# Kernel optimization log

Measured on AMD Instinct MI355X. Metric: run time of the kernel, lower is better.

## Reference

```python
import jax, jax.numpy as jnp
import numpy as np

COST_CLASS, COST_BBOX, COST_GIOU = 1.0, 5.0, 2.0
NUM_FRAMES, Q_PER_FRAME, NUM_TGT, NUM_CLASSES = 36, 100, 20, 92
B = 64


def box_cxcywh_to_xyxy(b):
    cx, cy, w, h = b[..., 0], b[..., 1], b[..., 2], b[..., 3]
    return jnp.stack([cx - 0.5 * w, cy - 0.5 * h, cx + 0.5 * w, cy + 0.5 * h], axis=-1)


def pairwise_giou(b1, b2):
    # b1: [..., Q, 4], b2: [..., T, 4], xyxy -> giou [..., Q, T]
    area1 = (b1[..., 2] - b1[..., 0]) * (b1[..., 3] - b1[..., 1])
    area2 = (b2[..., 2] - b2[..., 0]) * (b2[..., 3] - b2[..., 1])
    lt = jnp.maximum(b1[..., :, None, :2], b2[..., None, :, :2])
    rb = jnp.minimum(b1[..., :, None, 2:], b2[..., None, :, 2:])
    wh = jnp.clip(rb - lt, 0.0)
    inter = wh[..., 0] * wh[..., 1]
    union = area1[..., :, None] + area2[..., None, :] - inter
    iou = inter / union
    lt_e = jnp.minimum(b1[..., :, None, :2], b2[..., None, :, :2])
    rb_e = jnp.maximum(b1[..., :, None, 2:], b2[..., None, :, 2:])
    wh_e = jnp.clip(rb_e - lt_e, 0.0)
    area_e = wh_e[..., 0] * wh_e[..., 1]
    return iou - (area_e - union) / area_e


def compute_cost(pred_logits, pred_boxes, tgt_labels, tgt_boxes):
    b = pred_logits.shape[0]
    prob = jax.nn.softmax(pred_logits.reshape(b, NUM_FRAMES, Q_PER_FRAME, -1), axis=-1)  # [B,F,Q,C]
    pb = pred_boxes.reshape(b, NUM_FRAMES, Q_PER_FRAME, 4)
    lab = jnp.transpose(tgt_labels, (1, 0, 2))            # [B,F,T]
    tb = jnp.transpose(tgt_boxes, (1, 0, 2, 3))           # [B,F,T,4]
    onehot = jax.nn.one_hot(lab, prob.shape[-1], dtype=prob.dtype)  # [B,F,T,C]
    cost_class = -jnp.einsum('bfqc,bftc->bfqt', prob, onehot)
    cost_bbox = jnp.abs(pb[:, :, :, None, :] - tb[:, :, None, :, :]).sum(-1)  # L1 cdist
    giou = pairwise_giou(box_cxcywh_to_xyxy(pb), box_cxcywh_to_xyxy(tb))
    return COST_CLASS * cost_class + COST_BBOX * cost_bbox - COST_GIOU * giou


def auction_assign(cost):
    # cost [Q, T]; returns obj_of [T]: query index assigned to each target.
    # eps-optimal auction algorithm (replaces scipy linear_sum_assignment).
    Q, T = cost.shape
    benefit = -cost.T  # [T, Q]
    spread = jnp.max(benefit) - jnp.min(benefit) + 1e-6
    eps = spread / 1000.0
    neg_inf = jnp.asarray(-1e30, cost.dtype)

    def cond(s):
        _, _, obj_of, it = s
        return jnp.logical_and(jnp.any(obj_of < 0), it < 20000)

    def body(s):
        price, owner, obj_of, it = s
        unassigned = obj_of < 0                       # [T]
        vals = benefit - price[None, :]               # [T, Q]
        top2v, top2i = jax.lax.top_k(vals, 2)
        best_obj = top2i[:, 0]                        # [T]
        bid = price[best_obj] + (top2v[:, 0] - top2v[:, 1]) + eps
        bid = jnp.where(unassigned, bid, neg_inf)
        best_bid = jnp.full((Q,), neg_inf, cost.dtype).at[best_obj].max(bid)
        pids = jnp.arange(T, dtype=jnp.int32)
        win = unassigned & (bid >= best_bid[best_obj])
        winner = jnp.full((Q,), T, jnp.int32).at[best_obj].min(jnp.where(win, pids, T))
        has_bid = winner < T
        # evict previous owners of objects that received a bid
        evict = jnp.where(has_bid & (owner >= 0), owner, T)
        obj_of = obj_of.at[evict].set(-1, mode='drop')
        qids = jnp.arange(Q, dtype=jnp.int32)
        obj_of = obj_of.at[jnp.where(has_bid, winner, T)].set(jnp.where(has_bid, qids, -1), mode='drop')
        price = jnp.where(has_bid, best_bid, price)
        owner = jnp.where(has_bid, winner, owner)
        return price, owner, obj_of, it + 1

    init = (jnp.zeros((Q,), cost.dtype), jnp.full((Q,), -1, jnp.int32),
            jnp.full((T,), -1, jnp.int32), jnp.int32(0))
    _, _, obj_of, _ = jax.lax.while_loop(cond, body, init)
    return obj_of


def setup_inputs() -> dict:
    key = jax.random.key(0)
    k1, k2, k3, k4 = jax.random.split(key, 4)
    pred_logits = jax.random.normal(k1, (B, NUM_FRAMES * Q_PER_FRAME, NUM_CLASSES), jnp.float32)
    pred_boxes = jax.random.uniform(k2, (B, NUM_FRAMES * Q_PER_FRAME, 4), jnp.float32)
    tgt_labels = jax.random.randint(k3, (NUM_FRAMES, B, NUM_TGT), 0, NUM_CLASSES, jnp.int32)
    tgt_boxes = jax.random.uniform(k4, (NUM_FRAMES, B, NUM_TGT, 4), jnp.float32)
    return {'pred_logits': pred_logits, 'pred_boxes': pred_boxes,
            'tgt_labels': tgt_labels, 'tgt_boxes': tgt_boxes}


def reference(pred_logits, pred_boxes, tgt_labels, tgt_boxes):
    cost = compute_cost(pred_logits, pred_boxes, tgt_labels, tgt_boxes)  # [B,F,Q,T]
    b, f, q, t = cost.shape
    obj_of = jax.vmap(auction_assign)(cost.reshape(b * f, q, t))  # [BF, T]
    order = jnp.argsort(obj_of, axis=-1)  # scipy returns rows ascending
    pred_idx = jnp.take_along_axis(obj_of, order, axis=-1).reshape(b, f, t)
    tgt_idx = order.astype(jnp.int32).reshape(b, f, t)
    return cost, pred_idx, tgt_idx
```

## Files before the change

kernel.cpp:

```cpp
#include <hip/hip_runtime.h>

#define NF 36
#define QN 100
#define TN 20
#define CN 92
#define NB 64
#define BSTR 112

#define TOP2_STEP(VV, IDX) do { \
    float v_ = (VV); bool c_ = v_ > v0; \
    float nv1_ = __builtin_amdgcn_fmed3f(v_, v0, v1); \
    i0 = c_ ? (IDX) : i0; v0 = fmaxf(v0, v_); v1 = nv1_; } while (0)

__global__ __launch_bounds__(64) void matcher_kernel(
    const float* __restrict__ logits,
    const float* __restrict__ pboxes,
    const int*   __restrict__ tlabels,
    const float* __restrict__ tboxes,
    float* __restrict__ out_cost,
    float* __restrict__ out_pred,
    float* __restrict__ out_tgt)
{
    const int bf = blockIdx.x;
    const int b  = bf / NF;
    const int f  = bf % NF;
    const int lane = threadIdx.x;

    __shared__ __align__(16) float ben[TN][BSTR];
    __shared__ __align__(16) float price[BSTR];
    __shared__ int   owner[QN];
    __shared__ int   bbmax[QN];
    __shared__ int   wmin[QN];
    __shared__ int   evict[TN];
    __shared__ int   objl[TN];
    __shared__ int   slab[TN];
    __shared__ float tbr[TN][4];
    __shared__ float tbx[TN][4];
    __shared__ float tarea[TN];

    if (lane < TN) {
        const int base = (f * NB + b) * TN + lane;
        slab[lane] = tlabels[base];
        const float* tb = tboxes + (size_t)base * 4;
        float cx = tb[0], cy = tb[1], w = tb[2], h = tb[3];
        tbr[lane][0] = cx; tbr[lane][1] = cy; tbr[lane][2] = w; tbr[lane][3] = h;
        float x1 = cx - 0.5f * w, y1 = cy - 0.5f * h;
        float x2 = cx + 0.5f * w, y2 = cy + 0.5f * h;
        tbx[lane][0] = x1; tbx[lane][1] = y1; tbx[lane][2] = x2; tbx[lane][3] = y2;
        tarea[lane] = (x2 - x1) * (y2 - y1);
        evict[lane] = 0;
    }
    __syncthreads();

    float mn = INFINITY, mx = -INFINITY;
    for (int p = 0; p < 2; ++p) {
        const int q = lane + 64 * p;
        if (q < QN) {
            const size_t row = (size_t)b * (NF * QN) + (size_t)f * QN + q;
            const float* L = logits + row * CN;
            const float4* L4 = reinterpret_cast<const float4*>(L);

            float g[TN];
            #pragma unroll
            for (int t = 0; t < TN; ++t) g[t] = L[slab[t]];

            float m = -INFINITY, s = 0.f;
            #pragma unroll
            for (int i = 0; i < 23; ++i) {
                float4 v = L4[i];
                float cm = fmaxf(fmaxf(v.x, v.y), fmaxf(v.z, v.w));
                float m2 = fmaxf(m, cm);
                s = s * expf(m - m2)
                  + expf(v.x - m2) + expf(v.y - m2)
                  + expf(v.z - m2) + expf(v.w - m2);
                m = m2;
            }

            float4 pbv = reinterpret_cast<const float4*>(pboxes)[row];
            float cx = pbv.x, cy = pbv.y, w = pbv.z, h = pbv.w;
            float px1 = cx - 0.5f * w, py1 = cy - 0.5f * h;
            float px2 = cx + 0.5f * w, py2 = cy + 0.5f * h;
            float a1 = (px2 - px1) * (py2 - py1);

            for (int t = 0; t < TN; ++t) {
                float pc = expf(g[t] - m) / s;
                float cb = fabsf(cx - tbr[t][0]) + fabsf(cy - tbr[t][1]);
                cb = cb + fabsf(w - tbr[t][2]);
                cb = cb + fabsf(h - tbr[t][3]);
                float ltx = fmaxf(px1, tbx[t][0]), lty = fmaxf(py1, tbx[t][1]);
                float rbx = fminf(px2, tbx[t][2]), rby = fminf(py2, tbx[t][3]);
                float wx = fmaxf(rbx - ltx, 0.f), wy = fmaxf(rby - lty, 0.f);
                float inter = wx * wy;
                float uni = a1 + tarea[t] - inter;
                float iou = inter / uni;
                float ex1 = fminf(px1, tbx[t][0]), ey1 = fminf(py1, tbx[t][1]);
                float ex2 = fmaxf(px2, tbx[t][2]), ey2 = fmaxf(py2, tbx[t][3]);
                float ew = fmaxf(ex2 - ex1, 0.f), eh = fmaxf(ey2 - ey1, 0.f);
                float ae = ew * eh;
                float giou = iou - (ae - uni) / ae;
                float cost = (-pc) + 5.0f * cb - 2.0f * giou;
                ben[t][q] = -cost;
                mn = fminf(mn, cost);
                mx = fmaxf(mx, cost);
            }
        }
    }

    for (int i = lane; i < BSTR; i += 64) price[i] = 0.f;
    for (int i = lane; i < QN; i += 64) owner[i] = -1;
    if (lane < TN) {
        float4 ninf; ninf.x = ninf.y = ninf.z = ninf.w = -INFINITY;
        float4* sp = reinterpret_cast<float4*>(&ben[lane][100]);
        sp[0] = ninf; sp[1] = ninf; sp[2] = ninf;
    }
    __syncthreads();

    #pragma unroll
    for (int off = 32; off > 0; off >>= 1) {
        mn = fminf(mn, __shfl_xor(mn, off, 64));
        mx = fmaxf(mx, __shfl_xor(mx, off, 64));
    }
    const float eps = (((-mn) - (-mx)) + 1e-6f) / 1000.0f;

    {
        float4* dst = reinterpret_cast<float4*>(out_cost + (size_t)bf * (QN * TN));
        for (int i = lane; i < (QN * TN) / 4; i += 64) {
            int k = i * 4;
            int q = k / TN, t0 = k - q * TN;
            float4 v;
            v.x = -ben[t0 + 0][q]; v.y = -ben[t0 + 1][q];
            v.z = -ben[t0 + 2][q]; v.w = -ben[t0 + 3][q];
            dst[i] = v;
        }
    }

    const int myt = lane / 3;
    const int jj  = lane - myt * 3;
    const int q0  = jj * 36;
    const bool is_leader = (lane < 60) && (jj == 0);
    float4 breg4[9];
    {
        const int tt = (lane < 60) ? myt : 0;
        const float4* bp = reinterpret_cast<const float4*>(&ben[tt][q0]);
        #pragma unroll
        for (int k = 0; k < 9; ++k) breg4[k] = bp[k];
    }
    int myobj = -1;

    for (int it = 0; it < 20000; ++it) {
        unsigned long long U = __ballot(is_leader && (myobj < 0));
        if (U == 0ull) break;
        const int u = __popcll(U);

        int bidq = 0; float bidf = 0.f;
        if (u > 2) {
            float v0 = -INFINITY, v1 = -INFINITY; int i0 = q0;
            const float4* pp = reinterpret_cast<const float4*>(&price[q0]);
            #pragma unroll
            for (int k = 0; k < 9; ++k) {
                float4 bv = breg4[k];
                float4 pv = pp[k];
                TOP2_STEP(bv.x - pv.x, q0 + 4*k + 0);
                TOP2_STEP(bv.y - pv.y, q0 + 4*k + 1);
                TOP2_STEP(bv.z - pv.z, q0 + 4*k + 2);
                TOP2_STEP(bv.w - pv.w, q0 + 4*k + 3);
            }
            {
                float av0 = __shfl_down(v0, 1), av1 = __shfl_down(v1, 1);
                int   ai0 = __shfl_down(i0, 1);
                float bv0 = __shfl_down(v0, 2), bv1 = __shfl_down(v1, 2);
                int   bi0 = __shfl_down(i0, 2);
                if (av0 > v0) { v1 = fmaxf(v0, av1); v0 = av0; i0 = ai0; }
                else          { v1 = fmaxf(av0, v1); }
                if (bv0 > v0) { v1 = fmaxf(v0, bv1); v0 = bv0; i0 = bi0; }
                else          { v1 = fmaxf(bv0, v1); }
            }
            bidq = i0;
            bidf = price[i0] + (v0 - v1) + eps;
        } else {
            const int ta = (int)__builtin_ctzll(U) / 3;
            const int tb = (u == 2) ? (int)__builtin_ctzll(U & (U - 1ull)) / 3 : ta;
            const int grp = lane >> 5;
            const int tg  = grp ? tb : ta;
            const int l   = lane & 31;
            const int lc  = (l > 25) ? 25 : l;
            const int qb  = lc * 4;
            float4 bv = *reinterpret_cast<const float4*>(&ben[tg][qb]);
            float4 pv = *reinterpret_cast<const float4*>(&price[qb]);
            float v0 = -INFINITY, v1 = -INFINITY; int i0 = qb;
            TOP2_STEP(bv.x - pv.x, qb + 0);
            TOP2_STEP(bv.y - pv.y, qb + 1);
            TOP2_STEP(bv.z - pv.z, qb + 2);
            TOP2_STEP(bv.w - pv.w, qb + 3);
            #pragma unroll
            for (int s = 16; s >= 1; s >>= 1) {
                float av0 = __shfl_xor(v0, s), av1 = __shfl_xor(v1, s);
                int   ai0 = __shfl_xor(i0, s);
                bool take = (av0 > v0) || (av0 == v0 && ai0 < i0);
                float nv1 = take ? fmaxf(v0, av1) : fmaxf(v1, av0);
                v0 = take ? av0 : v0;
                i0 = take ? ai0 : i0;
                v1 = nv1;
            }
            float bidg = price[i0] + (v0 - v1) + eps;
            float b0 = __shfl(bidg, 0),  b1 = __shfl(bidg, 32);
            int   i0a = __shfl(i0, 0),   i0b = __shfl(i0, 32);
            if (lane == 3 * ta)            { bidq = i0a; bidf = b0; }
            if (u == 2 && lane == 3 * tb)  { bidq = i0b; bidf = b1; }
        }

        const bool act = is_leader && (myobj < 0);
        bool win = false;
        if (u == 1) {
            win = act;
        } else {
            if (act) { bbmax[bidq] = 0; wmin[bidq] = 64; }
            __syncthreads();
            if (act) atomicMax(&bbmax[bidq], __float_as_int(bidf));
            __syncthreads();
            bool cand = false;
            if (act) {
                cand = (__float_as_int(bidf) >= bbmax[bidq]);
                if (cand) atomicMin(&wmin[bidq], myt);
            }
            __syncthreads();
            win = cand && (wmin[bidq] == myt);
        }
        if (win) {
            int old = owner[bidq];
            owner[bidq] = myt;
            price[bidq] = bidf;
            myobj = bidq;
            if (old >= 0) evict[old] = 1;
        }
        __syncthreads();
        if (is_leader && evict[myt]) { myobj = -1; evict[myt] = 0; }
    }
    __syncthreads();
    if (is_leader) objl[myt] = myobj;
    __syncthreads();

    if (lane < TN) {
        int v = objl[lane];
        int r = 0;
        for (int u2 = 0; u2 < TN; ++u2) {
            int w = objl[u2];
            r += (w < v) || (w == v && u2 < lane);
        }
        out_pred[(size_t)bf * TN + r] = (float)v;
        out_tgt[(size_t)bf * TN + r]  = (float)lane;
    }
}

extern "C" void kernel_launch(void* const* d_in, const int* in_sizes, int n_in,
                              void* d_out, int out_size, void* d_ws, size_t ws_size,
                              hipStream_t stream) {
    const float* logits  = (const float*)d_in[0];
    const float* pboxes  = (const float*)d_in[1];
    const int*   tlabels = (const int*)d_in[2];
    const float* tboxes  = (const float*)d_in[3];

    float* out = (float*)d_out;
    float* out_cost = out;
    float* out_pred = out + (size_t)NB * NF * QN * TN;
    float* out_tgt  = out_pred + (size_t)NB * NF * TN;

    hipLaunchKernelGGL(matcher_kernel, dim3(NB * NF), dim3(64), 0, stream,
                       logits, pboxes, tlabels, tboxes, out_cost, out_pred, out_tgt);
}
```

Measured before the change: 176.6 us.

## Resolve auction bid conflicts with wave readlane scans instead of LDS atomics

Result: slower. 180.3 us (+2.1%).

```diff
diff --git a/kernel.cpp b/kernel.cpp
--- a/kernel.cpp
+++ b/kernel.cpp
@@ -7,10 +7,11 @@
 #define NB 64
 #define BSTR 112
 
-#define TOP2_STEP(VV, IDX) do { \
-    float v_ = (VV); bool c_ = v_ > v0; \
+#define TOP2P(BV, PV, IDX) do { \
+    float v_ = (BV) - (PV); bool c_ = v_ > v0; \
     float nv1_ = __builtin_amdgcn_fmed3f(v_, v0, v1); \
-    i0 = c_ ? (IDX) : i0; v0 = fmaxf(v0, v_); v1 = nv1_; } while (0)
+    i0 = c_ ? (IDX) : i0; p0 = c_ ? (PV) : p0; \
+    v0 = fmaxf(v0, v_); v1 = nv1_; } while (0)
 
 __global__ __launch_bounds__(64) void matcher_kernel(
     const float* __restrict__ logits,
@@ -28,10 +29,6 @@
 
     __shared__ __align__(16) float ben[TN][BSTR];
     __shared__ __align__(16) float price[BSTR];
-    __shared__ int   owner[QN];
-    __shared__ int   bbmax[QN];
-    __shared__ int   wmin[QN];
-    __shared__ int   evict[TN];
     __shared__ int   objl[TN];
     __shared__ int   slab[TN];
     __shared__ float tbr[TN][4];
@@ -48,7 +45,6 @@
         float x2 = cx + 0.5f * w, y2 = cy + 0.5f * h;
         tbx[lane][0] = x1; tbx[lane][1] = y1; tbx[lane][2] = x2; tbx[lane][3] = y2;
         tarea[lane] = (x2 - x1) * (y2 - y1);
-        evict[lane] = 0;
     }
     __syncthreads();
 
@@ -107,7 +103,6 @@
     }
 
     for (int i = lane; i < BSTR; i += 64) price[i] = 0.f;
-    for (int i = lane; i < QN; i += 64) owner[i] = -1;
     if (lane < TN) {
         float4 ninf; ninf.x = ninf.y = ninf.z = ninf.w = -INFINITY;
         float4* sp = reinterpret_cast<float4*>(&ben[lane][100]);
@@ -154,29 +149,29 @@
 
         int bidq = 0; float bidf = 0.f;
         if (u > 2) {
-            float v0 = -INFINITY, v1 = -INFINITY; int i0 = q0;
+            float v0 = -INFINITY, v1 = -INFINITY, p0 = 0.f; int i0 = q0;
             const float4* pp = reinterpret_cast<const float4*>(&price[q0]);
             #pragma unroll
             for (int k = 0; k < 9; ++k) {
                 float4 bv = breg4[k];
                 float4 pv = pp[k];
-                TOP2_STEP(bv.x - pv.x, q0 + 4*k + 0);
-                TOP2_STEP(bv.y - pv.y, q0 + 4*k + 1);
-                TOP2_STEP(bv.z - pv.z, q0 + 4*k + 2);
-                TOP2_STEP(bv.w - pv.w, q0 + 4*k + 3);
+                TOP2P(bv.x, pv.x, q0 + 4*k + 0);
+                TOP2P(bv.y, pv.y, q0 + 4*k + 1);
+                TOP2P(bv.z, pv.z, q0 + 4*k + 2);
+                TOP2P(bv.w, pv.w, q0 + 4*k + 3);
             }
             {
-                float av0 = __shfl_down(v0, 1), av1 = __shfl_down(v1, 1);
+                float av0 = __shfl_down(v0, 1), av1 = __shfl_down(v1, 1), ap0 = __shfl_down(p0, 1);
                 int   ai0 = __shfl_down(i0, 1);
-                float bv0 = __shfl_down(v0, 2), bv1 = __shfl_down(v1, 2);
+                float bv0 = __shfl_down(v0, 2), bv1 = __shfl_down(v1, 2), bp0 = __shfl_down(p0, 2);
                 int   bi0 = __shfl_down(i0, 2);
-                if (av0 > v0) { v1 = fmaxf(v0, av1); v0 = av0; i0 = ai0; }
+                if (av0 > v0) { v1 = fmaxf(v0, av1); v0 = av0; i0 = ai0; p0 = ap0; }
                 else          { v1 = fmaxf(av0, v1); }
-                if (bv0 > v0) { v1 = fmaxf(v0, bv1); v0 = bv0; i0 = bi0; }
+                if (bv0 > v0) { v1 = fmaxf(v0, bv1); v0 = bv0; i0 = bi0; p0 = bp0; }
                 else          { v1 = fmaxf(bv0, v1); }
             }
             bidq = i0;
-            bidf = price[i0] + (v0 - v1) + eps;
+            bidf = p0 + (v0 - v1) + eps;
         } else {
             const int ta = (int)__builtin_ctzll(U) / 3;
             const int tb = (u == 2) ? (int)__builtin_ctzll(U & (U - 1ull)) / 3 : ta;
@@ -187,22 +182,23 @@
             const int qb  = lc * 4;
             float4 bv = *reinterpret_cast<const float4*>(&ben[tg][qb]);
             float4 pv = *reinterpret_cast<const float4*>(&price[qb]);
-            float v0 = -INFINITY, v1 = -INFINITY; int i0 = qb;
-            TOP2_STEP(bv.x - pv.x, qb + 0);
-            TOP2_STEP(bv.y - pv.y, qb + 1);
-            TOP2_STEP(bv.z - pv.z, qb + 2);
-            TOP2_STEP(bv.w - pv.w, qb + 3);
+            float v0 = -INFINITY, v1 = -INFINITY, p0 = 0.f; int i0 = qb;
+            TOP2P(bv.x, pv.x, qb + 0);
+            TOP2P(bv.y, pv.y, qb + 1);
+            TOP2P(bv.z, pv.z, qb + 2);
+            TOP2P(bv.w, pv.w, qb + 3);
             #pragma unroll
             for (int s = 16; s >= 1; s >>= 1) {
-                float av0 = __shfl_xor(v0, s), av1 = __shfl_xor(v1, s);
+                float av0 = __shfl_xor(v0, s), av1 = __shfl_xor(v1, s), ap0 = __shfl_xor(p0, s);
                 int   ai0 = __shfl_xor(i0, s);
                 bool take = (av0 > v0) || (av0 == v0 && ai0 < i0);
                 float nv1 = take ? fmaxf(v0, av1) : fmaxf(v1, av0);
                 v0 = take ? av0 : v0;
                 i0 = take ? ai0 : i0;
+                p0 = take ? ap0 : p0;
                 v1 = nv1;
             }
-            float bidg = price[i0] + (v0 - v1) + eps;
+            float bidg = p0 + (v0 - v1) + eps;
             float b0 = __shfl(bidg, 0),  b1 = __shfl(bidg, 32);
             int   i0a = __shfl(i0, 0),   i0b = __shfl(i0, 32);
             if (lane == 3 * ta)            { bidq = i0a; bidf = b0; }
@@ -210,31 +206,24 @@
         }
 
         const bool act = is_leader && (myobj < 0);
-        bool win = false;
-        if (u == 1) {
-            win = act;
-        } else {
-            if (act) { bbmax[bidq] = 0; wmin[bidq] = 64; }
-            __syncthreads();
-            if (act) atomicMax(&bbmax[bidq], __float_as_int(bidf));
-            __syncthreads();
-            bool cand = false;
-            if (act) {
-                cand = (__float_as_int(bidf) >= bbmax[bidq]);
-                if (cand) atomicMin(&wmin[bidq], myt);
-            }
-            __syncthreads();
-            win = cand && (wmin[bidq] == myt);
-        }
-        if (win) {
-            int old = owner[bidq];
-            owner[bidq] = myt;
+        bool lose = false, ev = false;
+        {
+            unsigned long long uu = U;
+            while (uu) {
+                const int pos = (int)__builtin_ctzll(uu); uu &= uu - 1ull;
+                const int t2  = pos / 3;
+                const int   q2 = __builtin_amdgcn_readlane(bidq, pos);
+                const float f2 = __int_as_float(__builtin_amdgcn_readlane(__float_as_int(bidf), pos));
+                lose = lose || ((q2 == bidq) && ((f2 > bidf) || ((f2 == bidf) && (t2 < myt))));
+                ev   = ev   || (q2 == myobj);
+            }
+        }
+        if (act && !lose) {
+            myobj = bidq;
             price[bidq] = bidf;
-            myobj = bidq;
-            if (old >= 0) evict[old] = 1;
-        }
-        __syncthreads();
-        if (is_leader && evict[myt]) { myobj = -1; evict[myt] = 0; }
+        } else if (ev) {
+            myobj = -1;
+        }
     }
     __syncthreads();
     if (is_leader) objl[myt] = myobj;
```
